# Kernel tuning notes

Hardware: AMD Instinct MI355X
Metric: run time of the kernel (lower is better)

## Reference

```python
import jax, jax.numpy as jnp
import numpy as np

N, S, E, H = 8, 1024, 1024, 16
DK = E // H

def setup_inputs() -> dict:
    key = jax.random.key(0)
    ks = jax.random.split(key, 10)
    s = 1.0 / np.sqrt(E)
    x = jax.random.normal(ks[0], (N, S, E), dtype=jnp.float32)
    attn_mask = jax.random.randint(ks[1], (N, S, S), 0, 2) == 1
    Wq = jax.random.normal(ks[2], (E, E), dtype=jnp.float32) * s
    Wk = jax.random.normal(ks[3], (E, E), dtype=jnp.float32) * s
    Wv = jax.random.normal(ks[4], (E, E), dtype=jnp.float32) * s
    Wo = jax.random.normal(ks[5], (E, E), dtype=jnp.float32) * s
    bq = jax.random.normal(ks[6], (E,), dtype=jnp.float32) * s
    bk = jax.random.normal(ks[7], (E,), dtype=jnp.float32) * s
    bv = jax.random.normal(ks[8], (E,), dtype=jnp.float32) * s
    bo = jax.random.normal(ks[9], (E,), dtype=jnp.float32) * s
    return {"x": x, "attn_mask": attn_mask, "Wq": Wq, "bq": bq, "Wk": Wk, "bk": bk,
            "Wv": Wv, "bv": bv, "Wo": Wo, "bo": bo}

def reference(x, attn_mask, Wq, bq, Wk, bk, Wv, bv, Wo, bo):
    n, s, e = x.shape
    # projections, split into heads: (N, H, S, DK)
    q = (x @ Wq + bq).reshape(n, s, H, DK).transpose(0, 2, 1, 3)
    k = (x @ Wk + bk).reshape(n, s, H, DK).transpose(0, 2, 1, 3)
    v = (x @ Wv + bv).reshape(n, s, H, DK).transpose(0, 2, 1, 3)
    logits = jnp.einsum("nhqd,nhkd->nhqk", q, k) / np.sqrt(DK).astype(np.float32)
    # mask==True positions are suppressed (masked_fill with -1e9)
    logits = jnp.where(attn_mask[:, None, :, :], jnp.float32(-1e9), logits)
    attn = jax.nn.softmax(logits, axis=-1)  # exp(log_softmax) == softmax
    o = jnp.einsum("nhqk,nhkd->nhqd", attn, v)
    o = o.transpose(0, 2, 1, 3).reshape(n, s, e)
    return o @ Wo + bo
```

## Files before the change

kernel.cpp:

```cpp
#include <hip/hip_runtime.h>
#include <hip/hip_bf16.h>

typedef unsigned short u16;
typedef unsigned int   u32;
typedef unsigned long long u64;

#define SEQ 1024
#define EMB 1024
#define NH  16
#define DKH 64

#define QSCALE 0.18033688f
#define SCLAMP 43.3f

typedef __attribute__((ext_vector_type(8))) short short8;
typedef __attribute__((ext_vector_type(4))) float floatx4;

__device__ __forceinline__ float b2f(u16 u) {
  return __uint_as_float(((u32)u) << 16);
}
__device__ __forceinline__ u16 f2b(float f) {
  u32 u = __float_as_uint(f);
  u32 r = u + 0x7fffu + ((u >> 16) & 1u);
  return (u16)(r >> 16);
}

__device__ __forceinline__ void glds16(const u16* g, u16* l) {
  __builtin_amdgcn_global_load_lds(
      (const __attribute__((address_space(1))) u32*)g,
      (__attribute__((address_space(3))) u32*)l, 16, 0, 0);
}

__global__ __launch_bounds__(256) void probe_inputs(const u32* __restrict__ A,
                                                    const u32* __restrict__ B,
                                                    int* __restrict__ flags) {
  __shared__ int mA, mB, mBig, xB16;
  if (threadIdx.x == 0) { mA = 0; mB = 0; mBig = 0; xB16 = 0; }
  __syncthreads();
  int la = 0, lb = 0;
  for (int i = threadIdx.x; i < 4096; i += 256) {
    if ((A[i] & 0xFEFEFEFEu) == 0) la++;
    if ((B[i] & 0xFEFEFEFEu) == 0) lb++;
  }
  atomicAdd(&mA, la); atomicAdd(&mB, lb);
  __syncthreads();
  const int xIsB = (mA > mB) ? 1 : 0;
  const u32* X = xIsB ? B : A;
  const u32* M = xIsB ? A : B;
  int big = 0, cnt = 0;
  for (int i = threadIdx.x; i < 4096; i += 256)
    if (M[i] > 1u) big = 1;
  for (int i = threadIdx.x; i < 2048; i += 256) {
    u16 v = (u16)(X[i] & 0xffffu);
    int e = (v >> 7) & 0xFF;
    if (e >= 110 && e <= 135) cnt++;
  }
  if (big) atomicOr(&mBig, 1);
  atomicAdd(&xB16, cnt);
  __syncthreads();
  if (threadIdx.x == 0) {
    flags[0] = xIsB;
    flags[1] = (xB16 > 1500) ? 1 : 0;
    flags[2] = mBig;
  }
}

__global__ __launch_bounds__(256) void convert_x(const void* __restrict__ bigA,
                                                 const void* __restrict__ bigB,
                                                 const int* __restrict__ flags,
                                                 u16* __restrict__ out) {
  const void* x = flags[0] ? bigB : bigA;
  int i = (blockIdx.x * 256 + threadIdx.x) * 4;
  if (flags[1]) {
    *(ushort4*)(out + i) = *(const ushort4*)((const u16*)x + i);
  } else {
    float4 v = *(const float4*)((const float*)x + i);
    ushort4 o;
    o.x = f2b(v.x); o.y = f2b(v.y); o.z = f2b(v.z); o.w = f2b(v.w);
    *(ushort4*)(out + i) = o;
  }
}

__global__ __launch_bounds__(256) void build_maskbits(const void* __restrict__ bigA,
                                                      const void* __restrict__ bigB,
                                                      const int* __restrict__ flags,
                                                      u32* __restrict__ out) {
  const void* mask = flags[0] ? bigA : bigB;
  const int mbyte = flags[2];
  const int t = threadIdx.x;
  const int lane = t & 63, w = t >> 6;
  const u64 base0 = (u64)blockIdx.x * 8192;
#pragma unroll 4
  for (int k = 0; k < 32; k++) {
    u64 idx = base0 + k * 256 + t;
    int v;
    if (mbyte) v = ((const unsigned char*)mask)[idx] == 0;
    else       v = ((const u32*)mask)[idx] == 0;
    u64 b = __ballot(v);
    if (lane == 0) {
      u64 wbase = (base0 + k * 256 + w * 64) >> 5;
      out[wbase]     = (u32)b;
      out[wbase + 1] = (u32)(b >> 32);
    }
  }
}

__global__ __launch_bounds__(256) void transpose_convert_w4(
    const void* __restrict__ w0, const void* __restrict__ w1,
    const void* __restrict__ w2, const void* __restrict__ w3,
    u16* __restrict__ outQKV, u16* __restrict__ outO,
    const int* __restrict__ flags) {
  __shared__ float tile[32][33];
  const int z = blockIdx.z;
  const void* in = (z == 0) ? w0 : (z == 1) ? w1 : (z == 2) ? w2 : w3;
  u16* out = (z < 3) ? (outQKV + (u64)z * EMB * EMB) : outO;
  const float scale = (z == 0) ? QSCALE : 1.0f;
  const int amode = flags[1];
  const int tx = threadIdx.x & 31;
  const int ty = threadIdx.x >> 5;
  const int bx = blockIdx.x * 32, by = blockIdx.y * 32;
  if (amode) {
    const u16* inb = (const u16*)in;
#pragma unroll
    for (int r = ty; r < 32; r += 8)
      tile[r][tx] = b2f(inb[(u64)(by + r) * EMB + bx + tx]);
  } else {
    const float* inf = (const float*)in;
#pragma unroll
    for (int r = ty; r < 32; r += 8)
      tile[r][tx] = inf[(u64)(by + r) * EMB + bx + tx];
  }
  __syncthreads();
#pragma unroll
  for (int r = ty; r < 32; r += 8)
    out[(u64)(bx + r) * EMB + by + tx] = f2b(tile[tx][r] * scale);
}

__global__ __launch_bounds__(256) void convert_biases(const void* b0, const void* b1,
                                                      const void* b2, const void* b3,
                                                      float* __restrict__ out,
                                                      const int* __restrict__ flags) {
  const void* ptrs[4] = {b0, b1, b2, b3};
  const void* p = ptrs[blockIdx.x];
  const float scale = (blockIdx.x == 0) ? QSCALE : 1.0f;
  const int amode = flags[1];
  for (int i = threadIdx.x; i < 1024; i += 256) {
    float v = amode ? b2f(((const u16*)p)[i]) : ((const float*)p)[i];
    out[blockIdx.x * 1024 + i] = v * scale;
  }
}

#define VTP 65
__global__ __launch_bounds__(256) void transpose_v(const u16* __restrict__ in,
                                                   u16* __restrict__ out) {
  __shared__ u16 tile[64 * VTP];
  const int t = threadIdx.x;
  const int s0 = blockIdx.x * 64;
  const u64 off = (u64)blockIdx.y * SEQ * DKH;
  const int row = t >> 2, c0 = (t & 3) * 16;
  const u16* ip = in + off + (u64)(s0 + row) * DKH + c0;
  *(uint4*)(&tile[row * VTP + c0])     = *(const uint4*)(ip);
  *(uint4*)(&tile[row * VTP + c0 + 8]) = *(const uint4*)(ip + 8);
  __syncthreads();
  const int d = t >> 2;
  u16 buf[16];
#pragma unroll
  for (int j = 0; j < 16; j++) buf[j] = tile[(c0 + j) * VTP + d];
  u16* op = out + off + (u64)d * SEQ + s0 + c0;
  *(uint4*)(op)     = *(uint4*)(&buf[0]);
  *(uint4*)(op + 8) = *(uint4*)(&buf[8]);
}

__global__ __launch_bounds__(256) void gemm_qkv(
    const u16* __restrict__ X, const u16* __restrict__ Wt,
    const float* __restrict__ bias,
    u16* __restrict__ Qg, u16* __restrict__ Kg, u16* __restrict__ Vh,
    int row0) {
  __shared__ u16 As[128 * 32];
  __shared__ u16 Bs[128 * 32];
  const int t = threadIdx.x;
  const int lane = t & 63;
  const int w4 = t >> 6;
  const int wm = w4 >> 1, wn = w4 & 1;
  const int bM = blockIdx.x * 128, bN = blockIdx.y * 128;
  const int l15 = lane & 15, l4 = lane >> 4;

  floatx4 acc[4][4];
#pragma unroll
  for (int i = 0; i < 4; i++)
#pragma unroll
    for (int j = 0; j < 4; j++)
      acc[i][j] = (floatx4){0.f, 0.f, 0.f, 0.f};

  const int rb = w4 * 32 + (lane >> 2);
  const int cb = (lane & 3) * 8;
  const u16* Ap = X + (u64)(row0 + bM + rb) * EMB + cb;
  const u16* Bp = Wt + (u64)(bN + rb) * EMB + cb;
  u16* AsW = &As[(w4 * 32) * 32];
  u16* BsW = &Bs[(w4 * 32) * 32];

  for (int k0 = 0; k0 < EMB; k0 += 32) {
    __syncthreads();
    glds16(Ap + k0, AsW);
    glds16(Ap + 16 * EMB + k0, AsW + 512);
    glds16(Bp + k0, BsW);
    glds16(Bp + 16 * EMB + k0, BsW + 512);
    __syncthreads();
    short8 af[4], bfr[4];
#pragma unroll
    for (int i = 0; i < 4; i++) {
      af[i]  = *(const short8*)(&As[(wm * 64 + i * 16 + l15) * 32 + l4 * 8]);
      bfr[i] = *(const short8*)(&Bs[(wn * 64 + i * 16 + l15) * 32 + l4 * 8]);
    }
#pragma unroll
    for (int i = 0; i < 4; i++)
#pragma unroll
      for (int j = 0; j < 4; j++)
        acc[i][j] = __builtin_amdgcn_mfma_f32_16x16x32_bf16(af[i], bfr[j], acc[i][j], 0, 0, 0);
  }

  const int sec = bN >> 10;
  u16* outp = (sec == 0) ? Qg : (sec == 1) ? Kg : Vh;
#pragma unroll
  for (int j = 0; j < 4; j++) {
    int col = bN + wn * 64 + j * 16 + l15;
    float bv = bias[col];
    int colh = col & 1023;
    int h = colh >> 6, d = colh & 63;
#pragma unroll
    for (int i = 0; i < 4; i++) {
#pragma unroll
      for (int r = 0; r < 4; r++) {
        int row = bM + wm * 64 + i * 16 + l4 * 4 + r;
        float v = acc[i][j][r] + bv;
        int n = row >> 10, s = row & 1023;
        outp[((u64)((n * NH + h) * SEQ + s)) * DKH + d] = f2b(v);
      }
    }
  }
}

__global__ __launch_bounds__(256) void gemm_out(
    const u16* __restrict__ X, const u16* __restrict__ Wt,
    const float* __restrict__ bias, float* __restrict__ out) {
  __shared__ u16 As[128 * 32];
  __shared__ u16 Bs[128 * 32];
  const int t = threadIdx.x;
  const int lane = t & 63;
  const int w4 = t >> 6;
  const int wm = w4 >> 1, wn = w4 & 1;
  const int bM = blockIdx.x * 128, bN = blockIdx.y * 128;
  const int l15 = lane & 15, l4 = lane >> 4;

  floatx4 acc[4][4];
#pragma unroll
  for (int i = 0; i < 4; i++)
#pragma unroll
    for (int j = 0; j < 4; j++)
      acc[i][j] = (floatx4){0.f, 0.f, 0.f, 0.f};

  const int rb = w4 * 32 + (lane >> 2);
  const int cb = (lane & 3) * 8;
  const u16* Ap = X + (u64)(bM + rb) * EMB + cb;
  const u16* Bp = Wt + (u64)(bN + rb) * EMB + cb;
  u16* AsW = &As[(w4 * 32) * 32];
  u16* BsW = &Bs[(w4 * 32) * 32];

  for (int k0 = 0; k0 < EMB; k0 += 32) {
    __syncthreads();
    glds16(Ap + k0, AsW);
    glds16(Ap + 16 * EMB + k0, AsW + 512);
    glds16(Bp + k0, BsW);
    glds16(Bp + 16 * EMB + k0, BsW + 512);
    __syncthreads();
    short8 af[4], bfr[4];
#pragma unroll
    for (int i = 0; i < 4; i++) {
      af[i]  = *(const short8*)(&As[(wm * 64 + i * 16 + l15) * 32 + l4 * 8]);
      bfr[i] = *(const short8*)(&Bs[(wn * 64 + i * 16 + l15) * 32 + l4 * 8]);
    }
#pragma unroll
    for (int i = 0; i < 4; i++)
#pragma unroll
      for (int j = 0; j < 4; j++)
        acc[i][j] = __builtin_amdgcn_mfma_f32_16x16x32_bf16(af[i], bfr[j], acc[i][j], 0, 0, 0);
  }

#pragma unroll
  for (int j = 0; j < 4; j++) {
    int col = bN + wn * 64 + j * 16 + l15;
    float bv = bias[col];
#pragma unroll
    for (int i = 0; i < 4; i++) {
#pragma unroll
      for (int r = 0; r < 4; r++) {
        int row = bM + wm * 64 + i * 16 + l4 * 4 + r;
        out[(u64)row * EMB + col] = acc[i][j][r] + bv;
      }
    }
  }
}

__global__ __launch_bounds__(512, 6) void attn_mfma(
    const u16* __restrict__ Q, const u16* __restrict__ K,
    const u16* __restrict__ Vt, const u32* __restrict__ maskbits,
    int b0, u16* __restrict__ ctx) {
  __shared__ __align__(16) u16 Ks[2][64 * 64];
  __shared__ __align__(16) u16 Vs[2][64 * 64];
  __shared__ __align__(16) u16 Ps[128 * 64];

  const int t = threadIdx.x;
  const int lane = t & 63, w = t >> 6;
  const int l15 = lane & 15, l4 = lane >> 4;
  const int bid = blockIdx.x;
  const int h = bid & 15;
  const int qt = (bid >> 4) & 7;
  const int n = bid >> 7;
  const int nh = n * NH + h;
  const int q0 = qt * 128;
  const u64 hoff = (u64)nh * SEQ * DKH;

  const int r7 = l15 & 7;
  const int cA = (l4 ^ r7) << 3;
  const int cB = (l4 ^ r7 ^ 4) << 3;

  const int rt = w * 8 + (lane >> 3);
  const int chk = ((lane & 7) ^ (lane >> 3)) << 3;
  const u16* Kp = K + hoff + (u64)rt * DKH + chk;
  const u16* Vp = Vt + hoff + (u64)rt * SEQ + chk;
  const int ldsO = w * 512;

  short8 qf0, qf1;
  {
    const u16* qp = Q + hoff + (u64)(q0 + w * 16 + l15) * DKH + l4 * 8;
    qf0 = *(const short8*)(qp);
    qf1 = *(const short8*)(qp + 32);
  }

  short8 ones;
#pragma unroll
  for (int e = 0; e < 8; e++) ones[e] = (short)0x3F80;

  floatx4 o[4];
#pragma unroll
  for (int j = 0; j < 4; j++) o[j] = (floatx4){0.f, 0.f, 0.f, 0.f};
  floatx4 osum = (floatx4){0.f, 0.f, 0.f, 0.f};

  const u64 mrow = ((u64)((b0 + n) * SEQ + q0 + w * 16 + l15)) * 32;
  const int pq = w * 16 + l15;
  const int pc0 = (l4 * 4) ^ (r7 << 3);

  glds16(Kp, &Ks[0][ldsO]);
  glds16(Vp, &Vs[0][ldsO]);
  __syncthreads();

  int cur = 0;
  for (int kc = 0; kc < SEQ; kc += 64) {
    if (kc + 64 < SEQ) {
      const int nb = cur ^ 1;
      glds16(Kp + (kc + 64) * DKH, &Ks[nb][ldsO]);
      glds16(Vp + (kc + 64), &Vs[nb][ldsO]);
    }
    const u64 mbits = *(const u64*)(maskbits + mrow + (kc >> 5));
    const u16* Kc = &Ks[cur][0];
    const u16* Vc = &Vs[cur][0];

    __builtin_amdgcn_s_setprio(1);
#pragma unroll
    for (int j = 0; j < 4; j++) {
      floatx4 s = (floatx4){0.f, 0.f, 0.f, 0.f};
      const int rb = (j * 16 + l15) * 64;
      short8 kb0 = *(const short8*)(&Kc[rb + cA]);
      short8 kb1 = *(const short8*)(&Kc[rb + cB]);
      s = __builtin_amdgcn_mfma_f32_16x16x32_bf16(kb0, qf0, s, 0, 0, 0);
      s = __builtin_amdgcn_mfma_f32_16x16x32_bf16(kb1, qf1, s, 0, 0, 0);

      const u32 mj = (u32)(mbits >> (j * 16 + l4 * 4));
      float p0 = __uint_as_float(
          __float_as_uint(__builtin_amdgcn_exp2f(fminf(s[0], SCLAMP))) &
          (u32)__builtin_amdgcn_sbfe(mj, 0, 1));
      float p1 = __uint_as_float(
          __float_as_uint(__builtin_amdgcn_exp2f(fminf(s[1], SCLAMP))) &
          (u32)__builtin_amdgcn_sbfe(mj, 1, 1));
      float p2 = __uint_as_float(
          __float_as_uint(__builtin_amdgcn_exp2f(fminf(s[2], SCLAMP))) &
          (u32)__builtin_amdgcn_sbfe(mj, 2, 1));
      float p3 = __uint_as_float(
          __float_as_uint(__builtin_amdgcn_exp2f(fminf(s[3], SCLAMP))) &
          (u32)__builtin_amdgcn_sbfe(mj, 3, 1));

      uint2 pk;
      asm("v_cvt_pk_bf16_f32 %0, %1, %2" : "=v"(pk.x) : "v"(p0), "v"(p1));
      asm("v_cvt_pk_bf16_f32 %0, %1, %2" : "=v"(pk.y) : "v"(p2), "v"(p3));
      *(uint2*)(&Ps[pq * 64 + ((j * 16) ^ pc0)]) = pk;
    }

    short8 pa0 = *(const short8*)(&Ps[pq * 64 + cA]);
    short8 pa1 = *(const short8*)(&Ps[pq * 64 + cB]);
#pragma unroll
    for (int j = 0; j < 4; j++) {
      const int rb = (j * 16 + l15) * 64;
      short8 vb0 = *(const short8*)(&Vc[rb + cA]);
      short8 vb1 = *(const short8*)(&Vc[rb + cB]);
      o[j] = __builtin_amdgcn_mfma_f32_16x16x32_bf16(pa0, vb0, o[j], 0, 0, 0);
      o[j] = __builtin_amdgcn_mfma_f32_16x16x32_bf16(pa1, vb1, o[j], 0, 0, 0);
    }
    osum = __builtin_amdgcn_mfma_f32_16x16x32_bf16(pa0, ones, osum, 0, 0, 0);
    osum = __builtin_amdgcn_mfma_f32_16x16x32_bf16(pa1, ones, osum, 0, 0, 0);
    __builtin_amdgcn_s_setprio(0);

    __syncthreads();
    cur ^= 1;
  }

#pragma unroll
  for (int r = 0; r < 4; r++) {
    float invr = 1.0f / fmaxf(osum[r], 1e-30f);
    int q = q0 + w * 16 + l4 * 4 + r;
    u64 base = ((u64)(n * SEQ + q)) * EMB + h * DKH + l15;
#pragma unroll
    for (int j = 0; j < 4; j++)
      ctx[base + j * 16] = f2b(o[j][r] * invr);
  }
}

extern "C" void kernel_launch(void* const* d_in, const int* in_sizes, int n_in,
                              void* d_out, int out_size, void* d_ws, size_t ws_size,
                              hipStream_t stream) {
  int bigI[2] = {0, 1}, wI[4] = {2, 4, 6, 8}, bI[4] = {3, 5, 7, 9};
  int nb = 0, nw = 0, nbi = 0;
  for (int i = 0; i < n_in; i++) {
    if (in_sizes[i] == 8388608) { if (nb < 2) bigI[nb++] = i; }
    else if (in_sizes[i] == 1048576) { if (nw < 4) wI[nw++] = i; }
    else if (in_sizes[i] == 1024) { if (nbi < 4) bI[nbi++] = i; }
  }
  int oq = 0, ok = 1, ov = 2, oo = 3;
  if (nb == 2 && bigI[0] == 4 && bigI[1] == 9) { oq = 2; ok = 0; ov = 3; oo = 1; }

  const void* bigA = d_in[bigI[0]];
  const void* bigB = d_in[bigI[1]];
  const void* Wq = d_in[wI[oq]];
  const void* Wk = d_in[wI[ok]];
  const void* Wv = d_in[wI[ov]];
  const void* Wo = d_in[wI[oo]];
  const void* bq = d_in[bI[oq]];
  const void* bk = d_in[bI[ok]];
  const void* bv = d_in[bI[ov]];
  const void* bo = d_in[bI[oo]];

  char* ws = (char*)d_ws;
  u16* WtQKV = (u16*)ws;
  u16* WtO   = (u16*)(ws + (6ull << 20));
  float* biasf = (float*)(ws + (8ull << 20));
  int* flags = (int*)(ws + (8ull << 20) + 16384);
  u32* maskbits = (u32*)(ws + (8ull << 20) + 65536);
  u16* xb = (u16*)(ws + (10ull << 20));
  char* grp = ws + (26ull << 20);

  int G = 1;
  for (int g = 8; g >= 1; g >>= 1) {
    if (ws_size >= (26ull << 20) + (u64)g * (8ull << 20)) { G = g; break; }
  }
  const u64 gsz = (u64)G * (2ull << 20);
  u16* Qg = (u16*)grp;
  u16* Kg = (u16*)(grp + gsz);
  u16* Vh = (u16*)(grp + 2 * gsz);
  u16* Vt = (u16*)(grp + 3 * gsz);

  dim3 tb(256);

  probe_inputs<<<dim3(1), tb, 0, stream>>>((const u32*)bigA, (const u32*)bigB, flags);
  convert_x<<<dim3(8192), tb, 0, stream>>>(bigA, bigB, flags, xb);
  build_maskbits<<<dim3(1024), tb, 0, stream>>>(bigA, bigB, flags, maskbits);

  transpose_convert_w4<<<dim3(32, 32, 4), tb, 0, stream>>>(Wq, Wk, Wv, Wo, WtQKV, WtO, flags);
  convert_biases<<<dim3(4), tb, 0, stream>>>(bq, bk, bv, bo, biasf, flags);

  for (int b0 = 0; b0 < 8; b0 += G) {
    int row0 = b0 * 1024;
    gemm_qkv<<<dim3(8 * G, 24), tb, 0, stream>>>(xb, WtQKV, biasf, Qg, Kg, Vh, row0);
    transpose_v<<<dim3(16, G * 16), tb, 0, stream>>>(Vh, Vt);

    attn_mfma<<<dim3(G * 16 * 8), dim3(512), 0, stream>>>(Qg, Kg, Vt, maskbits, b0, Vh);

    gemm_out<<<dim3(8 * G, 8), tb, 0, stream>>>(Vh, WtO, biasf + 3072,
                                                (float*)d_out + (u64)row0 * EMB);
  }
}
```

Measured before the change: 335.8 us.

## Rewrite projection GEMMs with 256x128 tiles, double-buffered swizzled LDS, 512 threads

Both projection GEMMs now share a templated core that uses 256x128 block tiles with 8 waves, a K-step of 64, and a double-buffered LDS pipeline. Manual vmcnt waits and barriers let global-to-LDS loads for the next stage overlap MFMA compute on the current one. An XOR swizzle on the LDS chunk layout avoids bank conflicts, and s_setprio raises wave priority around the MFMA bursts. This targets the per-32-K double-sync stalls and low reuse of the old 128x128 kernels. The cost is fewer blocks per launch and a larger LDS footprint per block, about 96 KB.

```diff
diff --git a/kernel.cpp b/kernel.cpp
--- a/kernel.cpp
+++ b/kernel.cpp
@@ -171,134 +171,147 @@
   *(uint4*)(op + 8) = *(uint4*)(&buf[8]);
 }
 
-__global__ __launch_bounds__(256) void gemm_qkv(
+
+template <int OUTMODE>
+__device__ __forceinline__ void gemm_core(
+    const u16* __restrict__ X, const u16* __restrict__ Wt,
+    const float* __restrict__ bias,
+    u16* __restrict__ Qg, u16* __restrict__ Kg, u16* __restrict__ Vh,
+    float* __restrict__ outf, int row0) {
+  __shared__ __align__(16) u16 lds[2][(256 + 128) * 64];
+  const int t = threadIdx.x;
+  const int lane = t & 63;
+  const int w = t >> 6;
+  const int wr = w >> 1, wc = w & 1;
+  const int l15 = lane & 15, l4 = lane >> 4;
+  const int bM = blockIdx.x * 256, bN = blockIdx.y * 128;
+  const int r7 = l15 & 7;
+  const int cA = (l4 ^ r7) << 3;
+  const int cB = (l4 ^ r7 ^ 4) << 3;
+
+  floatx4 acc[4][4];
+#pragma unroll
+  for (int i = 0; i < 4; i++)
+#pragma unroll
+    for (int j = 0; j < 4; j++)
+      acc[i][j] = (floatx4){0.f, 0.f, 0.f, 0.f};
+
+  const int srow = w * 8 + (lane >> 3);
+  const int schk = ((lane & 7) ^ (lane >> 3)) << 3;
+  const u16* Ap = X + (u64)(row0 + bM + srow) * EMB + schk;
+  const u16* Bp = Wt + (u64)(bN + srow) * EMB + schk;
+  u16* Ad0 = &lds[0][w * 512];
+  u16* Bd0 = &lds[0][16384 + w * 512];
+  u16* Ad1 = &lds[1][w * 512];
+  u16* Bd1 = &lds[1][16384 + w * 512];
+
+  auto stage = [&](u16* Ad, u16* Bd, int k0) {
+    glds16(Ap + k0, Ad);
+    glds16(Ap + k0 + 64 * EMB, Ad + 4096);
+    glds16(Ap + k0 + 128 * EMB, Ad + 8192);
+    glds16(Ap + k0 + 192 * EMB, Ad + 12288);
+    glds16(Bp + k0, Bd);
+    glds16(Bp + k0 + 64 * EMB, Bd + 4096);
+  };
+
+  auto compute = [&](const u16* __restrict__ Ab, const u16* __restrict__ Bb) {
+    short8 bf[4][2];
+#pragma unroll
+    for (int n = 0; n < 4; n++) {
+      const int gr = (wc * 64 + n * 16 + l15) * 64;
+      bf[n][0] = *(const short8*)(&Bb[gr + cA]);
+      bf[n][1] = *(const short8*)(&Bb[gr + cB]);
+    }
+#pragma unroll
+    for (int mh = 0; mh < 2; mh++) {
+      short8 af[2][2];
+#pragma unroll
+      for (int m = 0; m < 2; m++) {
+        const int fr = (wr * 64 + mh * 32 + m * 16 + l15) * 64;
+        af[m][0] = *(const short8*)(&Ab[fr + cA]);
+        af[m][1] = *(const short8*)(&Ab[fr + cB]);
+      }
+      __builtin_amdgcn_s_setprio(1);
+#pragma unroll
+      for (int m = 0; m < 2; m++)
+#pragma unroll
+        for (int n = 0; n < 4; n++) {
+          acc[mh * 2 + m][n] = __builtin_amdgcn_mfma_f32_16x16x32_bf16(
+              af[m][0], bf[n][0], acc[mh * 2 + m][n], 0, 0, 0);
+          acc[mh * 2 + m][n] = __builtin_amdgcn_mfma_f32_16x16x32_bf16(
+              af[m][1], bf[n][1], acc[mh * 2 + m][n], 0, 0, 0);
+        }
+      __builtin_amdgcn_s_setprio(0);
+    }
+  };
+
+  stage(Ad0, Bd0, 0);
+  for (int k0 = 0; k0 < EMB; k0 += 128) {
+    stage(Ad1, Bd1, k0 + 64);
+    asm volatile("s_waitcnt vmcnt(6)" ::: "memory");
+    asm volatile("s_barrier" ::: "memory");
+    compute(&lds[0][0], &lds[0][16384]);
+    asm volatile("s_barrier" ::: "memory");
+    if (k0 + 128 < EMB) {
+      stage(Ad0, Bd0, k0 + 128);
+      asm volatile("s_waitcnt vmcnt(6)" ::: "memory");
+    } else {
+      asm volatile("s_waitcnt vmcnt(0)" ::: "memory");
+    }
+    asm volatile("s_barrier" ::: "memory");
+    compute(&lds[1][0], &lds[1][16384]);
+    asm volatile("s_barrier" ::: "memory");
+  }
+
+  if (OUTMODE == 0) {
+    const int sec = bN >> 10;
+    u16* outp = (sec == 0) ? Qg : (sec == 1) ? Kg : Vh;
+#pragma unroll
+    for (int n = 0; n < 4; n++) {
+      int col = bN + wc * 64 + n * 16 + l15;
+      float bv = bias[col];
+      int colh = col & 1023;
+      int h = colh >> 6, d = colh & 63;
+#pragma unroll
+      for (int mt = 0; mt < 4; mt++) {
+#pragma unroll
+        for (int r = 0; r < 4; r++) {
+          int row = bM + wr * 64 + mt * 16 + l4 * 4 + r;
+          float v = acc[mt][n][r] + bv;
+          int nb = row >> 10, s = row & 1023;
+          outp[((u64)((nb * NH + h) * SEQ + s)) * DKH + d] = f2b(v);
+        }
+      }
+    }
+  } else {
+#pragma unroll
+    for (int n = 0; n < 4; n++) {
+      int col = bN + wc * 64 + n * 16 + l15;
+      float bv = bias[col];
+#pragma unroll
+      for (int mt = 0; mt < 4; mt++) {
+#pragma unroll
+        for (int r = 0; r < 4; r++) {
+          int row = bM + wr * 64 + mt * 16 + l4 * 4 + r;
+          outf[(u64)row * EMB + col] = acc[mt][n][r] + bv;
+        }
+      }
+    }
+  }
+}
+
+__global__ __launch_bounds__(512, 2) void gemm_qkv(
     const u16* __restrict__ X, const u16* __restrict__ Wt,
     const float* __restrict__ bias,
     u16* __restrict__ Qg, u16* __restrict__ Kg, u16* __restrict__ Vh,
     int row0) {
-  __shared__ u16 As[128 * 32];
-  __shared__ u16 Bs[128 * 32];
-  const int t = threadIdx.x;
-  const int lane = t & 63;
-  const int w4 = t >> 6;
-  const int wm = w4 >> 1, wn = w4 & 1;
-  const int bM = blockIdx.x * 128, bN = blockIdx.y * 128;
-  const int l15 = lane & 15, l4 = lane >> 4;
-
-  floatx4 acc[4][4];
-#pragma unroll
-  for (int i = 0; i < 4; i++)
-#pragma unroll
-    for (int j = 0; j < 4; j++)
-      acc[i][j] = (floatx4){0.f, 0.f, 0.f, 0.f};
-
-  const int rb = w4 * 32 + (lane >> 2);
-  const int cb = (lane & 3) * 8;
-  const u16* Ap = X + (u64)(row0 + bM + rb) * EMB + cb;
-  const u16* Bp = Wt + (u64)(bN + rb) * EMB + cb;
-  u16* AsW = &As[(w4 * 32) * 32];
-  u16* BsW = &Bs[(w4 * 32) * 32];
-
-  for (int k0 = 0; k0 < EMB; k0 += 32) {
-    __syncthreads();
-    glds16(Ap + k0, AsW);
-    glds16(Ap + 16 * EMB + k0, AsW + 512);
-    glds16(Bp + k0, BsW);
-    glds16(Bp + 16 * EMB + k0, BsW + 512);
-    __syncthreads();
-    short8 af[4], bfr[4];
-#pragma unroll
-    for (int i = 0; i < 4; i++) {
-      af[i]  = *(const short8*)(&As[(wm * 64 + i * 16 + l15) * 32 + l4 * 8]);
-      bfr[i] = *(const short8*)(&Bs[(wn * 64 + i * 16 + l15) * 32 + l4 * 8]);
-    }
-#pragma unroll
-    for (int i = 0; i < 4; i++)
-#pragma unroll
-      for (int j = 0; j < 4; j++)
-        acc[i][j] = __builtin_amdgcn_mfma_f32_16x16x32_bf16(af[i], bfr[j], acc[i][j], 0, 0, 0);
-  }
-
-  const int sec = bN >> 10;
-  u16* outp = (sec == 0) ? Qg : (sec == 1) ? Kg : Vh;
-#pragma unroll
-  for (int j = 0; j < 4; j++) {
-    int col = bN + wn * 64 + j * 16 + l15;
-    float bv = bias[col];
-    int colh = col & 1023;
-    int h = colh >> 6, d = colh & 63;
-#pragma unroll
-    for (int i = 0; i < 4; i++) {
-#pragma unroll
-      for (int r = 0; r < 4; r++) {
-        int row = bM + wm * 64 + i * 16 + l4 * 4 + r;
-        float v = acc[i][j][r] + bv;
-        int n = row >> 10, s = row & 1023;
-        outp[((u64)((n * NH + h) * SEQ + s)) * DKH + d] = f2b(v);
-      }
-    }
-  }
-}
-
-__global__ __launch_bounds__(256) void gemm_out(
+  gemm_core<0>(X, Wt, bias, Qg, Kg, Vh, nullptr, row0);
+}
+
+__global__ __launch_bounds__(512, 2) void gemm_out(
     const u16* __restrict__ X, const u16* __restrict__ Wt,
     const float* __restrict__ bias, float* __restrict__ out) {
-  __shared__ u16 As[128 * 32];
-  __shared__ u16 Bs[128 * 32];
-  const int t = threadIdx.x;
-  const int lane = t & 63;
-  const int w4 = t >> 6;
-  const int wm = w4 >> 1, wn = w4 & 1;
-  const int bM = blockIdx.x * 128, bN = blockIdx.y * 128;
-  const int l15 = lane & 15, l4 = lane >> 4;
-
-  floatx4 acc[4][4];
-#pragma unroll
-  for (int i = 0; i < 4; i++)
-#pragma unroll
-    for (int j = 0; j < 4; j++)
-      acc[i][j] = (floatx4){0.f, 0.f, 0.f, 0.f};
-
-  const int rb = w4 * 32 + (lane >> 2);
-  const int cb = (lane & 3) * 8;
-  const u16* Ap = X + (u64)(bM + rb) * EMB + cb;
-  const u16* Bp = Wt + (u64)(bN + rb) * EMB + cb;
-  u16* AsW = &As[(w4 * 32) * 32];
-  u16* BsW = &Bs[(w4 * 32) * 32];
-
-  for (int k0 = 0; k0 < EMB; k0 += 32) {
-    __syncthreads();
-    glds16(Ap + k0, AsW);
-    glds16(Ap + 16 * EMB + k0, AsW + 512);
-    glds16(Bp + k0, BsW);
-    glds16(Bp + 16 * EMB + k0, BsW + 512);
-    __syncthreads();
-    short8 af[4], bfr[4];
-#pragma unroll
-    for (int i = 0; i < 4; i++) {
-      af[i]  = *(const short8*)(&As[(wm * 64 + i * 16 + l15) * 32 + l4 * 8]);
-      bfr[i] = *(const short8*)(&Bs[(wn * 64 + i * 16 + l15) * 32 + l4 * 8]);
-    }
-#pragma unroll
-    for (int i = 0; i < 4; i++)
-#pragma unroll
-      for (int j = 0; j < 4; j++)
-        acc[i][j] = __builtin_amdgcn_mfma_f32_16x16x32_bf16(af[i], bfr[j], acc[i][j], 0, 0, 0);
-  }
-
-#pragma unroll
-  for (int j = 0; j < 4; j++) {
-    int col = bN + wn * 64 + j * 16 + l15;
-    float bv = bias[col];
-#pragma unroll
-    for (int i = 0; i < 4; i++) {
-#pragma unroll
-      for (int r = 0; r < 4; r++) {
-        int row = bM + wm * 64 + i * 16 + l4 * 4 + r;
-        out[(u64)row * EMB + col] = acc[i][j][r] + bv;
-      }
-    }
-  }
+  gemm_core<1>(X, Wt, bias, nullptr, nullptr, nullptr, out, 0);
 }
 
 __global__ __launch_bounds__(512, 6) void attn_mfma(
@@ -478,12 +491,12 @@
 
   for (int b0 = 0; b0 < 8; b0 += G) {
     int row0 = b0 * 1024;
-    gemm_qkv<<<dim3(8 * G, 24), tb, 0, stream>>>(xb, WtQKV, biasf, Qg, Kg, Vh, row0);
+    gemm_qkv<<<dim3(4 * G, 24), dim3(512), 0, stream>>>(xb, WtQKV, biasf, Qg, Kg, Vh, row0);
     transpose_v<<<dim3(16, G * 16), tb, 0, stream>>>(Vh, Vt);
 
     attn_mfma<<<dim3(G * 16 * 8), dim3(512), 0, stream>>>(Qg, Kg, Vt, maskbits, b0, Vh);
 
-    gemm_out<<<dim3(8 * G, 8), tb, 0, stream>>>(Vh, WtO, biasf + 3072,
-                                                (float*)d_out + (u64)row0 * EMB);
-  }
-}
+    gemm_out<<<dim3(4 * G, 8), dim3(512), 0, stream>>>(Vh, WtO, biasf + 3072,
+                                                       (float*)d_out + (u64)row0 * EMB);
+  }
+}
```

Result: faster. 322.0 us (-4.1%).
